# Kernel tuning notes

Hardware: AMD Instinct MI355X
Metric: run time of the kernel (lower is better)

The kernel has to match this reference:

```python
import jax, jax.numpy as jnp
import numpy as np

B, P, C = 2, 2048, 64
SIZE = 128          # image_size
K = 8               # points_per_pixel (z-buffer depth)
RADIUS = 1.5        # in pixels
RAD_POW = 2
TAU = 1.0
BIG = 1e10          # sentinel z for pixels a point does not cover


def setup_inputs() -> dict:
    key = jax.random.key(0)
    k1, k2, k3 = jax.random.split(key, 3)
    xy = jax.random.uniform(k1, (B, P, 2), minval=-1.0, maxval=1.0)   # NDC xy
    z = jax.random.uniform(k2, (B, P, 1), minval=0.1, maxval=10.0)    # depth > 0
    pts3D = jnp.concatenate([xy, z], axis=-1)                          # [B,P,3]
    src = jax.random.normal(k3, (B, C, P), dtype=jnp.float32)          # [B,C,P]
    return {"pts3D": pts3D, "src": src}


def reference(pts3D, src):
    # --- sign flips from the torch forward: pts[:, :, :2] *= -1 ---
    pts = pts3D * jnp.array([-1.0, -1.0, 1.0], dtype=pts3D.dtype)
    px, py, pz = pts[..., 0], pts[..., 1], pts[..., 2]                 # [B,P]

    r_ndc = float(RADIUS) / float(SIZE) * 2.0

    # pixel-center NDC grid (pytorch3d convention: +x left, +y up)
    ii = jnp.arange(SIZE, dtype=pts.dtype)
    ndc = 1.0 - 2.0 * (ii + 0.5) / SIZE                                # [SIZE]

    # squared NDC distance pixel->point: [B,H,W,P]
    dx = ndc[None, None, :, None] - px[:, None, None, :]               # [B,1,W,P]
    dy = ndc[None, :, None, None] - py[:, None, None, :]               # [B,H,1,P]
    d2 = dx * dx + dy * dy                                             # [B,H,W,P]

    # rasterize_points: per pixel, K nearest-in-z points within radius
    inside = d2 <= r_ndc * r_ndc
    zkey = jnp.where(inside, pz[:, None, None, :], jnp.asarray(BIG, d2.dtype))
    neg_top, idx = jax.lax.top_k(-zkey, K)            # smallest z first, [B,H,W,K]
    valid = (-neg_top) < BIG                           # idx >= 0 equivalent

    dist = jnp.take_along_axis(d2, idx, axis=-1)       # [B,H,W,K]
    dist = dist / (r_ndc ** RAD_POW)

    # alphas = (1 - clamp(dist,0.001,1)^0.5)^tau
    alphas = (1.0 - jnp.sqrt(jnp.clip(dist, 0.001, 1.0))) ** TAU
    alphas = jnp.where(valid, alphas, 0.0)

    # alpha_composite: w_k = a_k * prod_{j<k} (1 - a_j), front-to-back
    T = jnp.cumprod(1.0 - alphas, axis=-1)
    w = alphas * jnp.concatenate([jnp.ones_like(T[..., :1]), T[..., :-1]], axis=-1)

    # gather features per batch: src [B,C,P], idx [B,H,W,K] -> [B,C,H,W,K]
    gathered = jax.vmap(lambda f, i: f[:, i])(src, idx)
    out = jnp.einsum('bchwk,bhwk->bchw', gathered, w)  # [B,C,H,W]
    return out
```

## Files before the change

### kernel.cpp

```cpp
#include <hip/hip_runtime.h>
#include <hip/hip_bf16.h>

#define BATCH 2
#define NPTS 2048
#define NCH 64
#define IMG 128
#define KTOP 8
#define BIGF 1e10f

__global__ __launch_bounds__(256) void transpose_src(
    const float* __restrict__ src, float* __restrict__ srcT) {
  __shared__ float tile[64][65];
  int b = blockIdx.x >> 5;
  int p0 = (blockIdx.x & 31) << 6;
  int tx = threadIdx.x & 63;
  int ty = threadIdx.x >> 6;
  const float* s = src + b * NCH * NPTS;
  #pragma unroll
  for (int cc = 0; cc < 64; cc += 4) {
    int c = cc + ty;
    tile[tx][c] = s[c * NPTS + p0 + tx];
  }
  __syncthreads();
  float* dT = srcT + (b * NPTS + p0) * NCH;
  #pragma unroll
  for (int pp = 0; pp < 64; pp += 4) {
    int p = pp + ty;
    dT[p * NCH + tx] = tile[p][tx];
  }
}

__global__ __launch_bounds__(64) void raster_composite(
    const float* __restrict__ pts,
    const float* __restrict__ srcT,
    float* __restrict__ out) {
  __shared__ float lx[NPTS], ly[NPTS], lz[NPTS];
  __shared__ int lidx[NPTS];
  __shared__ int cnt_s;

  const int bid = blockIdx.x;
  const int b = bid >> 8;
  const int h = (bid >> 1) & 127;
  const int w0 = (bid & 1) << 6;
  const int tid = threadIdx.x;

  if (tid == 0) cnt_s = 0;
  __syncthreads();

  const float r_ndc = 0.0234375f;
  const float r2 = r_ndc * r_ndc;
  const float yc = 1.0f - 2.0f * (h + 0.5f) / 128.0f;

  const float* pb = pts + b * NPTS * 3;
  for (int p = tid; p < NPTS; p += 64) {
    float py = pb[p * 3 + 1];
    float dy = yc + py;
    if (dy * dy <= r2) {
      int pos = atomicAdd(&cnt_s, 1);
      lx[pos] = pb[p * 3 + 0];
      ly[pos] = py;
      lz[pos] = pb[p * 3 + 2];
      lidx[pos] = p;
    }
  }
  __syncthreads();
  const int cnt = cnt_s;

  const int w = w0 + tid;
  const float xc = 1.0f - 2.0f * (w + 0.5f) / 128.0f;

  float bz[KTOP], bd[KTOP];
  int bi[KTOP];
  #pragma unroll
  for (int k = 0; k < KTOP; ++k) { bz[k] = BIGF; bd[k] = 0.f; bi[k] = 0x7fffffff; }

  for (int j = 0; j < cnt; ++j) {
    float dx = xc + lx[j];
    float dyy = yc + ly[j];
    float d2 = dx * dx + dyy * dyy;
    if (d2 <= r2) {
      float cz = lz[j], cd = d2;
      int ci = lidx[j];
      #pragma unroll
      for (int s = 0; s < KTOP; ++s) {
        bool lt = (cz < bz[s]) || (cz == bz[s] && ci < bi[s]);
        float tz = bz[s], td = bd[s];
        int ti = bi[s];
        if (lt) { bz[s] = cz; bd[s] = cd; bi[s] = ci; cz = tz; cd = td; ci = ti; }
      }
    }
  }

  float wgt[KTOP];
  float T = 1.0f;
  const float inv_r2 = 1.0f / r2;
  #pragma unroll
  for (int k = 0; k < KTOP; ++k) {
    float alpha = 0.0f;
    if (bz[k] < BIGF) {
      float dist = bd[k] * inv_r2;
      dist = fminf(fmaxf(dist, 0.001f), 1.0f);
      alpha = 1.0f - sqrtf(dist);
    } else {
      bi[k] = 0;
    }
    wgt[k] = alpha * T;
    T *= (1.0f - alpha);
  }

  const float4* sb = (const float4*)(srcT + b * NPTS * NCH);
  const float4* rows[KTOP];
  #pragma unroll
  for (int k = 0; k < KTOP; ++k) rows[k] = sb + bi[k] * (NCH / 4);

  float* ob = out + (b * NCH * IMG + h) * IMG + w;
  for (int cq = 0; cq < NCH / 4; ++cq) {
    float4 acc = {0.f, 0.f, 0.f, 0.f};
    #pragma unroll
    for (int k = 0; k < KTOP; ++k) {
      float4 v = rows[k][cq];
      acc.x += wgt[k] * v.x;
      acc.y += wgt[k] * v.y;
      acc.z += wgt[k] * v.z;
      acc.w += wgt[k] * v.w;
    }
    int c = cq * 4;
    ob[(c + 0) * (IMG * IMG)] = acc.x;
    ob[(c + 1) * (IMG * IMG)] = acc.y;
    ob[(c + 2) * (IMG * IMG)] = acc.z;
    ob[(c + 3) * (IMG * IMG)] = acc.w;
  }
}

extern "C" void kernel_launch(void* const* d_in, const int* in_sizes, int n_in,
                              void* d_out, int out_size, void* d_ws, size_t ws_size,
                              hipStream_t stream) {
  const float* pts = (const float*)d_in[0];
  const float* src = (const float*)d_in[1];
  float* out = (float*)d_out;
  float* srcT = (float*)d_ws;

  transpose_src<<<BATCH * (NPTS / 64), 256, 0, stream>>>(src, srcT);
  raster_composite<<<BATCH * IMG * 2, 64, 0, stream>>>(pts, srcT, out);
}
```

Baseline: 95.41 us.

## Bin points into per-row buckets and split channel compositing across waves

Adds a bin_points kernel that uses global atomics to place each point into per-image-row buckets of packed float4 (x,y,z,idx). The raster kernel then loads only its row's candidates instead of every block scanning all 2048 points. The raster block grows to 256 threads: all four wavefronts redo the same top-K selection, then each writes 16 of the 64 channels. Costs are an extra memset and kernel launch, four-fold redundant top-K work, and a fixed cap of 256 candidates per row that silently drops points beyond it.

```diff
diff --git a/kernel.cpp b/kernel.cpp
--- a/kernel.cpp
+++ b/kernel.cpp
@@ -7,6 +7,7 @@
 #define IMG 128
 #define KTOP 8
 #define BIGF 1e10f
+#define CAP 256
 
 __global__ __launch_bounds__(256) void transpose_src(
     const float* __restrict__ src, float* __restrict__ srcT) {
@@ -30,13 +31,40 @@
   }
 }
 
-__global__ __launch_bounds__(64) void raster_composite(
+__global__ __launch_bounds__(256) void bin_points(
     const float* __restrict__ pts,
+    float4* __restrict__ bins,
+    int* __restrict__ counts) {
+  int g = blockIdx.x * 256 + threadIdx.x;
+  if (g >= BATCH * NPTS) return;
+  int b = g >> 11;
+  int p = g & (NPTS - 1);
+  const float* pp = pts + g * 3;
+  float x = pp[0], y = pp[1], z = pp[2];
+  const float r_ndc = 0.0234375f;
+  const float r2 = r_ndc * r_ndc;
+  float t = 1.0f + y;
+  int h0 = (int)floorf((t - r_ndc) * 64.0f - 0.5f);
+  int h1 = (int)ceilf((t + r_ndc) * 64.0f - 0.5f);
+  h0 = max(h0, 0);
+  h1 = min(h1, IMG - 1);
+  for (int h = h0; h <= h1; ++h) {
+    float yc = 1.0f - 2.0f * (h + 0.5f) / 128.0f;
+    float dy = yc + y;
+    if (dy * dy <= r2) {
+      int pos = atomicAdd(&counts[b * IMG + h], 1);
+      if (pos < CAP)
+        bins[(b * IMG + h) * CAP + pos] = make_float4(x, y, z, __int_as_float(p));
+    }
+  }
+}
+
+__global__ __launch_bounds__(256) void raster_composite(
+    const float4* __restrict__ bins,
+    const int* __restrict__ counts,
     const float* __restrict__ srcT,
     float* __restrict__ out) {
-  __shared__ float lx[NPTS], ly[NPTS], lz[NPTS];
-  __shared__ int lidx[NPTS];
-  __shared__ int cnt_s;
+  __shared__ float4 cand[CAP];
 
   const int bid = blockIdx.x;
   const int b = bid >> 8;
@@ -44,29 +72,17 @@
   const int w0 = (bid & 1) << 6;
   const int tid = threadIdx.x;
 
-  if (tid == 0) cnt_s = 0;
+  const int cnt = min(counts[b * IMG + h], CAP);
+  const float4* grow = bins + (b * IMG + h) * CAP;
+  for (int j = tid; j < cnt; j += 256) cand[j] = grow[j];
   __syncthreads();
 
   const float r_ndc = 0.0234375f;
   const float r2 = r_ndc * r_ndc;
   const float yc = 1.0f - 2.0f * (h + 0.5f) / 128.0f;
 
-  const float* pb = pts + b * NPTS * 3;
-  for (int p = tid; p < NPTS; p += 64) {
-    float py = pb[p * 3 + 1];
-    float dy = yc + py;
-    if (dy * dy <= r2) {
-      int pos = atomicAdd(&cnt_s, 1);
-      lx[pos] = pb[p * 3 + 0];
-      ly[pos] = py;
-      lz[pos] = pb[p * 3 + 2];
-      lidx[pos] = p;
-    }
-  }
-  __syncthreads();
-  const int cnt = cnt_s;
-
-  const int w = w0 + tid;
+  const int pix = tid & 63;
+  const int w = w0 + pix;
   const float xc = 1.0f - 2.0f * (w + 0.5f) / 128.0f;
 
   float bz[KTOP], bd[KTOP];
@@ -75,12 +91,13 @@
   for (int k = 0; k < KTOP; ++k) { bz[k] = BIGF; bd[k] = 0.f; bi[k] = 0x7fffffff; }
 
   for (int j = 0; j < cnt; ++j) {
-    float dx = xc + lx[j];
-    float dyy = yc + ly[j];
+    float4 c4 = cand[j];
+    float dx = xc + c4.x;
+    float dyy = yc + c4.y;
     float d2 = dx * dx + dyy * dyy;
     if (d2 <= r2) {
-      float cz = lz[j], cd = d2;
-      int ci = lidx[j];
+      float cz = c4.z, cd = d2;
+      int ci = __float_as_int(c4.w);
       #pragma unroll
       for (int s = 0; s < KTOP; ++s) {
         bool lt = (cz < bz[s]) || (cz == bz[s] && ci < bi[s]);
@@ -113,8 +130,11 @@
   #pragma unroll
   for (int k = 0; k < KTOP; ++k) rows[k] = sb + bi[k] * (NCH / 4);
 
+  const int cq0 = (tid >> 6) * 4;
   float* ob = out + (b * NCH * IMG + h) * IMG + w;
-  for (int cq = 0; cq < NCH / 4; ++cq) {
+  #pragma unroll
+  for (int q = 0; q < 4; ++q) {
+    int cq = cq0 + q;
     float4 acc = {0.f, 0.f, 0.f, 0.f};
     #pragma unroll
     for (int k = 0; k < KTOP; ++k) {
@@ -138,8 +158,15 @@
   const float* pts = (const float*)d_in[0];
   const float* src = (const float*)d_in[1];
   float* out = (float*)d_out;
-  float* srcT = (float*)d_ws;
 
+  char* ws = (char*)d_ws;
+  float* srcT = (float*)ws;
+  float4* bins = (float4*)(ws + (size_t)(BATCH * NPTS * NCH) * 4);
+  int* counts = (int*)(ws + (size_t)(BATCH * NPTS * NCH) * 4 +
+                       (size_t)(BATCH * IMG * CAP) * 16);
+
+  hipMemsetAsync(counts, 0, BATCH * IMG * sizeof(int), stream);
   transpose_src<<<BATCH * (NPTS / 64), 256, 0, stream>>>(src, srcT);
-  raster_composite<<<BATCH * IMG * 2, 64, 0, stream>>>(pts, srcT, out);
+  bin_points<<<(BATCH * NPTS + 255) / 256, 256, 0, stream>>>(pts, bins, counts);
+  raster_composite<<<BATCH * IMG * 2, 256, 0, stream>>>(bins, counts, srcT, out);
 }
```

Measured after the change: 94.93 us. No clear change (-0.5%).

## Use 256-thread blocks splitting channel compositing across four warps, pack candidates

Applied to the files above, without the earlier changes.

Each block now runs 256 threads. Four wavefronts each redundantly compute the top-K for the same 64 pixels, then each wavefront composites a quarter of the channels. Candidate points are packed into a capped float4 shared array of 256 entries instead of four 2048-entry arrays, which cuts LDS use and speeds up the row-filter loop. The cap silently drops candidates if a row has more than 256 points, and the top-K selection is duplicated four times per block.

```diff
diff --git a/kernel.cpp b/kernel.cpp
--- a/kernel.cpp
+++ b/kernel.cpp
@@ -7,6 +7,7 @@
 #define IMG 128
 #define KTOP 8
 #define BIGF 1e10f
+#define CAP 256
 
 __global__ __launch_bounds__(256) void transpose_src(
     const float* __restrict__ src, float* __restrict__ srcT) {
@@ -30,12 +31,11 @@
   }
 }
 
-__global__ __launch_bounds__(64) void raster_composite(
+__global__ __launch_bounds__(256) void raster_fused(
     const float* __restrict__ pts,
     const float* __restrict__ srcT,
     float* __restrict__ out) {
-  __shared__ float lx[NPTS], ly[NPTS], lz[NPTS];
-  __shared__ int lidx[NPTS];
+  __shared__ float4 cand[CAP];
   __shared__ int cnt_s;
 
   const int bid = blockIdx.x;
@@ -52,21 +52,21 @@
   const float yc = 1.0f - 2.0f * (h + 0.5f) / 128.0f;
 
   const float* pb = pts + b * NPTS * 3;
-  for (int p = tid; p < NPTS; p += 64) {
-    float py = pb[p * 3 + 1];
-    float dy = yc + py;
+  for (int p = tid; p < NPTS; p += 256) {
+    float y = pb[p * 3 + 1];
+    float dy = yc + y;
     if (dy * dy <= r2) {
       int pos = atomicAdd(&cnt_s, 1);
-      lx[pos] = pb[p * 3 + 0];
-      ly[pos] = py;
-      lz[pos] = pb[p * 3 + 2];
-      lidx[pos] = p;
+      if (pos < CAP)
+        cand[pos] = make_float4(pb[p * 3 + 0], y, pb[p * 3 + 2],
+                                __int_as_float(p));
     }
   }
   __syncthreads();
-  const int cnt = cnt_s;
+  const int cnt = min(cnt_s, CAP);
 
-  const int w = w0 + tid;
+  const int pix = tid & 63;
+  const int w = w0 + pix;
   const float xc = 1.0f - 2.0f * (w + 0.5f) / 128.0f;
 
   float bz[KTOP], bd[KTOP];
@@ -75,12 +75,13 @@
   for (int k = 0; k < KTOP; ++k) { bz[k] = BIGF; bd[k] = 0.f; bi[k] = 0x7fffffff; }
 
   for (int j = 0; j < cnt; ++j) {
-    float dx = xc + lx[j];
-    float dyy = yc + ly[j];
+    float4 c4 = cand[j];
+    float dx = xc + c4.x;
+    float dyy = yc + c4.y;
     float d2 = dx * dx + dyy * dyy;
     if (d2 <= r2) {
-      float cz = lz[j], cd = d2;
-      int ci = lidx[j];
+      float cz = c4.z, cd = d2;
+      int ci = __float_as_int(c4.w);
       #pragma unroll
       for (int s = 0; s < KTOP; ++s) {
         bool lt = (cz < bz[s]) || (cz == bz[s] && ci < bi[s]);
@@ -113,8 +114,11 @@
   #pragma unroll
   for (int k = 0; k < KTOP; ++k) rows[k] = sb + bi[k] * (NCH / 4);
 
+  const int cq0 = (tid >> 6) * 4;
   float* ob = out + (b * NCH * IMG + h) * IMG + w;
-  for (int cq = 0; cq < NCH / 4; ++cq) {
+  #pragma unroll
+  for (int q = 0; q < 4; ++q) {
+    int cq = cq0 + q;
     float4 acc = {0.f, 0.f, 0.f, 0.f};
     #pragma unroll
     for (int k = 0; k < KTOP; ++k) {
@@ -141,5 +145,5 @@
   float* srcT = (float*)d_ws;
 
   transpose_src<<<BATCH * (NPTS / 64), 256, 0, stream>>>(src, srcT);
-  raster_composite<<<BATCH * IMG * 2, 64, 0, stream>>>(pts, srcT, out);
+  raster_fused<<<BATCH * IMG * 2, 256, 0, stream>>>(pts, srcT, out);
 }
```

After: 88.58 us. 1.08x faster.
